# Kernel tuning notes

Measured on AMD Instinct MI355X. Metric: run time of the kernel, lower is better.

Reference implementation:

```python
import jax, jax.numpy as jnp
import numpy as np

B = 1048576  # batch
A = 3        # number of actors in the ensemble


def _linear_params(key, out_d, in_d):
    """Stacked-over-actors torch.nn.Linear-style init: U(-1/sqrt(in), 1/sqrt(in))."""
    k1, k2 = jax.random.split(key)
    s = 1.0 / np.sqrt(in_d)
    W = jax.random.uniform(k1, (A, out_d, in_d), minval=-s, maxval=s, dtype=jnp.float32)
    b = jax.random.uniform(k2, (A, out_d), minval=-s, maxval=s, dtype=jnp.float32)
    return W, b


def setup_inputs() -> dict:
    key = jax.random.key(0)
    ks = jax.random.split(key, 10)
    spatial = jax.random.normal(ks[0], (B, 3, 9), dtype=jnp.float32)
    car_stats = jax.random.normal(ks[1], (B, 4), dtype=jnp.float32)  # unused by the model
    Wmx, bmx = _linear_params(ks[2], 10, 6)
    Wnx, bnx = _linear_params(ks[3], 10, 3)
    Wmy, bmy = _linear_params(ks[4], 10, 6)
    Wny, bny = _linear_params(ks[5], 10, 3)
    Wmz, bmz = _linear_params(ks[6], 5, 6)
    Wnz, bnz = _linear_params(ks[7], 5, 3)
    Wlin, blin = _linear_params(ks[8], 25, 25)
    Wout, bout = _linear_params(ks[9], 15, 25)
    return {
        "spatial": spatial, "car_stats": car_stats,
        "Wmx": Wmx, "bmx": bmx, "Wnx": Wnx, "bnx": bnx,
        "Wmy": Wmy, "bmy": bmy, "Wny": Wny, "bny": bny,
        "Wmz": Wmz, "bmz": bmz, "Wnz": Wnz, "bnz": bnz,
        "Wlin": Wlin, "blin": blin, "Wout": Wout, "bout": bout,
    }


def reference(spatial, car_stats,
              Wmx, bmx, Wnx, bnx,
              Wmy, bmy, Wny, bny,
              Wmz, bmz, Wnz, bnz,
              Wlin, blin, Wout, bout):
    # SimpleSpatialInput vectorized over the actor axis 'a':
    # (Linear(6->size)(s[:, :6])) * (Linear(3->size)(s[:, 6:9]))
    def proc(s, Wm, bm, Wn, bn):
        m = jnp.einsum('bi,aoi->bao', s[:, :6], Wm) + bm   # [B, A, size]
        n = jnp.einsum('bi,aoi->bao', s[:, 6:9], Wn) + bn  # [B, A, size]
        return m * n

    px = proc(spatial[:, 0], Wmx, bmx, Wnx, bnx)  # [B, A, 10]
    py = proc(spatial[:, 1], Wmy, bmy, Wny, bny)  # [B, A, 10]
    pz = proc(spatial[:, 2], Wmz, bmz, Wnz, bnz)  # [B, A, 5]
    ps = jnp.concatenate([px, py, pz], axis=-1)   # [B, A, 25]

    h = jnp.einsum('bad,aod->bao', ps, Wlin) + blin  # [B, A, 25]
    h = h / (1.0 + jnp.abs(h))                       # Softsign
    out = jnp.einsum('bad,aod->bao', h, Wout) + bout # [B, A, 15]

    result = jnp.transpose(out, (0, 2, 1))           # [B, 15, A] (stack dim=2)
    multiplier = jax.nn.softmax(result[:, 9, :], axis=1)  # [B, A]
    # stack of result[:, i] * multiplier over i=0..8, cumsum over actors,
    # take last -> plain weighted sum over the actor axis.
    return jnp.einsum('boa,ba->bo', result[:, :9, :], multiplier)  # [B, 9]
```

## Files before the change

### kernel.cpp

```cpp
#include <hip/hip_runtime.h>


typedef _Float16 half8  __attribute__((ext_vector_type(8)));
typedef float    floatx4 __attribute__((ext_vector_type(4)));

#define NFRAG 21
#define FRAG_HALFS (NFRAG * 512)
#define TPB 16

__global__ __launch_bounds__(256) void prep_frags(
    const float* __restrict__ Wmx, const float* __restrict__ bmx,
    const float* __restrict__ Wnx, const float* __restrict__ bnx,
    const float* __restrict__ Wmy, const float* __restrict__ bmy,
    const float* __restrict__ Wny, const float* __restrict__ bny,
    const float* __restrict__ Wmz, const float* __restrict__ bmz,
    const float* __restrict__ Wnz, const float* __restrict__ bnz,
    const float* __restrict__ Wlin, const float* __restrict__ blin,
    const float* __restrict__ Wout, const float* __restrict__ bout,
    _Float16* __restrict__ frag)
{
    int i = threadIdx.x + blockIdx.x * blockDim.x;
    if (i >= FRAG_HALFS) return;
    int f = i >> 9, rem = i & 511;
    int lane = rem >> 3, j = rem & 7;
    int q = lane >> 4, m = lane & 15;
    int a = f / 7, idx = f % 7;
    float v = 0.f;
    if (idx < 4) {
        int c = m + ((idx & 1) ? 16 : 0);
        int k = 8 * q + j;
        bool npart = (idx >= 2);
        if (c < 10) {
            if (!npart) { if (k < 6)             v = Wmx[(a*10 + c)*6 + k];
                          else if (k == 27)      v = bmx[a*10 + c]; }
            else        { if (k >= 6 && k < 9)   v = Wnx[(a*10 + c)*3 + (k-6)];
                          else if (k == 27)      v = bnx[a*10 + c]; }
        } else if (c < 20) {
            if (!npart) { if (k >= 9 && k < 15)  v = Wmy[(a*10 + c-10)*6 + (k-9)];
                          else if (k == 27)      v = bmy[a*10 + c-10]; }
            else        { if (k >= 15 && k < 18) v = Wny[(a*10 + c-10)*3 + (k-15)];
                          else if (k == 27)      v = bny[a*10 + c-10]; }
        } else if (c < 25) {
            if (!npart) { if (k >= 18 && k < 24) v = Wmz[(a*5 + c-20)*6 + (k-18)];
                          else if (k == 27)      v = bmz[a*5 + c-20]; }
            else        { if (k >= 24 && k < 27) v = Wnz[(a*5 + c-20)*3 + (k-24)];
                          else if (k == 27)      v = bnz[a*5 + c-20]; }
        }
    } else if (idx < 6) {
        int o  = m + ((idx == 5) ? 16 : 0);
        int kc = 16 * (j >> 2) + 4 * q + (j & 3);
        if (o < 25) {
            if (kc < 25)       v = Wlin[(a*25 + o)*25 + kc];
            else if (kc == 25) v = blin[a*25 + o];
        }
    } else {
        int ko = 16 * (j >> 2) + 4 * q + (j & 3);
        if (m < 10) {
            if (ko < 25)       v = Wout[(a*15 + m)*25 + ko];
            else if (ko == 25) v = bout[a*15 + m];
        }
    }
    frag[(size_t)f * 512 + lane * 8 + j] = (_Float16)v;
}

__global__ __launch_bounds__(256) void actor_mfma(
    const float* __restrict__ spatial,
    const _Float16* __restrict__ frag,
    float* __restrict__ out)
{
    __shared__ float lds_o[4 * 144];

    const int t = threadIdx.x;
    const int lane = t & 63, w = t >> 6;
    const int q = lane >> 4, e = lane & 15;
    const size_t b0 = (size_t)blockIdx.x * (64 * TPB);

    half8 F[NFRAG];
    #pragma unroll
    for (int f = 0; f < NFRAG; ++f)
        F[f] = *(const half8*)(frag + (size_t)f * 512 + lane * 8);
    #pragma unroll
    for (int f = 0; f < NFRAG; ++f)
        asm volatile("" : "+v"(F[f]));

    const float* sbase = spatial + (b0 + (size_t)(w * 16 + e)) * 27 + 8 * q;
    float* const ldso = lds_o + w * 144;
    const floatx4 z = {0.f, 0.f, 0.f, 0.f};

    auto loadT = [&](float (&dst)[8], int tt) {
        const float* s_ = sbase + (size_t)tt * (64 * 27);
        #pragma unroll
        for (int j = 0; j < 8; ++j) {
            int k = 8 * q + j;
            float v = (k == 27) ? 1.f : 0.f;
            if (k < 27) v = s_[j];
            dst[j] = v;
        }
    };

    auto tileCompute = [&](const float (&cur)[8], int tt) {
        half8 Bs;
        #pragma unroll
        for (int j = 0; j < 8; ++j) Bs[j] = (_Float16)cur[j];

        floatx4 oacc[3];
        #pragma unroll
        for (int a = 0; a < 3; ++a) {
            const int fb = a * 7;
            half8 P;
            {
                floatx4 M0 = __builtin_amdgcn_mfma_f32_16x16x32_f16(F[fb+0], Bs, z, 0,0,0);
                floatx4 N0 = __builtin_amdgcn_mfma_f32_16x16x32_f16(F[fb+2], Bs, z, 0,0,0);
                #pragma unroll
                for (int r = 0; r < 4; ++r) P[r] = (_Float16)(M0[r] * N0[r]);
            }
            {
                floatx4 M1 = __builtin_amdgcn_mfma_f32_16x16x32_f16(F[fb+1], Bs, z, 0,0,0);
                floatx4 N1 = __builtin_amdgcn_mfma_f32_16x16x32_f16(F[fb+3], Bs, z, 0,0,0);
                #pragma unroll
                for (int r = 0; r < 4; ++r) P[4 + r] = (_Float16)(M1[r] * N1[r]);
            }
            if (q == 2) P[5] = (_Float16)1.f;

            floatx4 H0 = __builtin_amdgcn_mfma_f32_16x16x32_f16(F[fb+4], P, z, 0,0,0);
            floatx4 H1 = __builtin_amdgcn_mfma_f32_16x16x32_f16(F[fb+5], P, z, 0,0,0);

            half8 Hh;
            #pragma unroll
            for (int r = 0; r < 4; ++r) {
                float v0 = H0[r];
                Hh[r]     = (_Float16)(v0 * __builtin_amdgcn_rcpf(1.0f + fabsf(v0)));
                float v1 = H1[r];
                Hh[4 + r] = (_Float16)(v1 * __builtin_amdgcn_rcpf(1.0f + fabsf(v1)));
            }
            if (q == 2) Hh[5] = (_Float16)1.f;

            oacc[a] = __builtin_amdgcn_mfma_f32_16x16x32_f16(F[fb+6], Hh, z, 0,0,0);
        }

        const int src9 = 32 + e;
        float g0 = __shfl(oacc[0][1], src9, 64);
        float g1 = __shfl(oacc[1][1], src9, 64);
        float g2 = __shfl(oacc[2][1], src9, 64);
        float mx = fmaxf(g0, fmaxf(g1, g2));
        float e0 = __expf(g0 - mx);
        float e1 = __expf(g1 - mx);
        float e2 = __expf(g2 - mx);
        float inv = __builtin_amdgcn_rcpf(e0 + e1 + e2);
        e0 *= inv; e1 *= inv; e2 *= inv;

        float res[4];
        #pragma unroll
        for (int r = 0; r < 4; ++r)
            res[r] = oacc[0][r] * e0 + oacc[1][r] * e1 + oacc[2][r] * e2;

        if (q < 2) {
            #pragma unroll
            for (int r = 0; r < 4; ++r) ldso[e * 9 + 4 * q + r] = res[r];
        } else if (q == 2) {
            ldso[e * 9 + 8] = res[0];
        }
        if (lane < 36) {
            float4 v = *(const float4*)(ldso + lane * 4);
            *(float4*)(out + (b0 + (size_t)tt * 64 + w * 16) * 9 + lane * 4) = v;
        }
    };

    float sA[8], sB[8];
    loadT(sA, 0);
    for (int tt = 0; tt < TPB; tt += 2) {
        loadT(sB, tt + 1);
        tileCompute(sA, tt);
        if (tt + 2 < TPB) loadT(sA, tt + 2);
        tileCompute(sB, tt + 1);
    }
}

extern "C" void kernel_launch(void* const* d_in, const int* in_sizes, int n_in,
                              void* d_out, int out_size, void* d_ws, size_t ws_size,
                              hipStream_t stream) {
    const float* spatial = (const float*)d_in[0];
    const float* Wmx  = (const float*)d_in[2];
    const float* bmx  = (const float*)d_in[3];
    const float* Wnx  = (const float*)d_in[4];
    const float* bnx  = (const float*)d_in[5];
    const float* Wmy  = (const float*)d_in[6];
    const float* bmy  = (const float*)d_in[7];
    const float* Wny  = (const float*)d_in[8];
    const float* bny  = (const float*)d_in[9];
    const float* Wmz  = (const float*)d_in[10];
    const float* bmz  = (const float*)d_in[11];
    const float* Wnz  = (const float*)d_in[12];
    const float* bnz  = (const float*)d_in[13];
    const float* Wlin = (const float*)d_in[14];
    const float* blin = (const float*)d_in[15];
    const float* Wout = (const float*)d_in[16];
    const float* bout = (const float*)d_in[17];
    float* out = (float*)d_out;

    _Float16* frag = (_Float16*)d_ws;

    prep_frags<<<dim3(42), dim3(256), 0, stream>>>(
        Wmx, bmx, Wnx, bnx, Wmy, bmy, Wny, bny, Wmz, bmz, Wnz, bnz,
        Wlin, blin, Wout, bout, frag);

    const int nb = in_sizes[0] / 27;
    dim3 grid(nb / (64 * TPB));
    actor_mfma<<<grid, dim3(256), 0, stream>>>(spatial, frag, out);
}
```

Measured before the change: 260.1 us.

## Stage weight fragments in LDS instead of registers and shrink tiles per block

The 21 weight fragments now live in shared memory: each block copies them cooperatively, and every wave reads them with LDS loads per MFMA instead of holding 84 VGPRs of fragments. This frees registers to raise occupancy and hide global-load latency. To compensate, tiles per block drop from 16 to 4, giving four times as many blocks. The cost is extra LDS traffic per tile and a per-block fragment copy plus barrier that is amortised over fewer tiles.

Result: faster. 241.2 us (-7.3%).

```diff
diff --git a/kernel.cpp b/kernel.cpp
--- a/kernel.cpp
+++ b/kernel.cpp
@@ -6,7 +6,7 @@
 
 #define NFRAG 21
 #define FRAG_HALFS (NFRAG * 512)
-#define TPB 16
+#define TPB 4
 
 __global__ __launch_bounds__(256) void prep_frags(
     const float* __restrict__ Wmx, const float* __restrict__ bmx,
@@ -68,33 +68,42 @@
     const _Float16* __restrict__ frag,
     float* __restrict__ out)
 {
-    __shared__ float lds_o[4 * 144];
+    __shared__ _Float16 lds_f[FRAG_HALFS];
+    __shared__ float    lds_o[4 * 144];
 
     const int t = threadIdx.x;
     const int lane = t & 63, w = t >> 6;
     const int q = lane >> 4, e = lane & 15;
     const size_t b0 = (size_t)blockIdx.x * (64 * TPB);
 
-    half8 F[NFRAG];
+    {
+        const float4* gf = (const float4*)frag;
+        float4* df = (float4*)lds_f;
+        #pragma unroll
+        for (int k = 0; k < 6; ++k) {
+            int idx = t + k * 256;
+            if (idx < 1344) df[idx] = gf[idx];
+        }
+    }
+
+    const float* sbase = spatial + (b0 + (size_t)(w * 16 + e)) * 27 + 8 * q;
+    float vbase[8];
     #pragma unroll
-    for (int f = 0; f < NFRAG; ++f)
-        F[f] = *(const half8*)(frag + (size_t)f * 512 + lane * 8);
-    #pragma unroll
-    for (int f = 0; f < NFRAG; ++f)
-        asm volatile("" : "+v"(F[f]));
-
-    const float* sbase = spatial + (b0 + (size_t)(w * 16 + e)) * 27 + 8 * q;
+    for (int j = 0; j < 8; ++j) vbase[j] = ((8 * q + j) == 27) ? 1.f : 0.f;
+
     float* const ldso = lds_o + w * 144;
     const floatx4 z = {0.f, 0.f, 0.f, 0.f};
 
+    __syncthreads();
+
+    int fo = lane;
+
     auto loadT = [&](float (&dst)[8], int tt) {
         const float* s_ = sbase + (size_t)tt * (64 * 27);
         #pragma unroll
         for (int j = 0; j < 8; ++j) {
             int k = 8 * q + j;
-            float v = (k == 27) ? 1.f : 0.f;
-            if (k < 27) v = s_[j];
-            dst[j] = v;
+            dst[j] = (k < 27) ? s_[j] : vbase[j];
         }
     };
 
@@ -106,24 +115,26 @@
         floatx4 oacc[3];
         #pragma unroll
         for (int a = 0; a < 3; ++a) {
+            asm volatile("" : "+v"(fo));
+            const half8* fp = (const half8*)lds_f + fo;
             const int fb = a * 7;
             half8 P;
             {
-                floatx4 M0 = __builtin_amdgcn_mfma_f32_16x16x32_f16(F[fb+0], Bs, z, 0,0,0);
-                floatx4 N0 = __builtin_amdgcn_mfma_f32_16x16x32_f16(F[fb+2], Bs, z, 0,0,0);
+                floatx4 M0 = __builtin_amdgcn_mfma_f32_16x16x32_f16(fp[(fb+0)*64], Bs, z, 0,0,0);
+                floatx4 N0 = __builtin_amdgcn_mfma_f32_16x16x32_f16(fp[(fb+2)*64], Bs, z, 0,0,0);
                 #pragma unroll
                 for (int r = 0; r < 4; ++r) P[r] = (_Float16)(M0[r] * N0[r]);
             }
             {
-                floatx4 M1 = __builtin_amdgcn_mfma_f32_16x16x32_f16(F[fb+1], Bs, z, 0,0,0);
-                floatx4 N1 = __builtin_amdgcn_mfma_f32_16x16x32_f16(F[fb+3], Bs, z, 0,0,0);
+                floatx4 M1 = __builtin_amdgcn_mfma_f32_16x16x32_f16(fp[(fb+1)*64], Bs, z, 0,0,0);
+                floatx4 N1 = __builtin_amdgcn_mfma_f32_16x16x32_f16(fp[(fb+3)*64], Bs, z, 0,0,0);
                 #pragma unroll
                 for (int r = 0; r < 4; ++r) P[4 + r] = (_Float16)(M1[r] * N1[r]);
             }
             if (q == 2) P[5] = (_Float16)1.f;
 
-            floatx4 H0 = __builtin_amdgcn_mfma_f32_16x16x32_f16(F[fb+4], P, z, 0,0,0);
-            floatx4 H1 = __builtin_amdgcn_mfma_f32_16x16x32_f16(F[fb+5], P, z, 0,0,0);
+            floatx4 H0 = __builtin_amdgcn_mfma_f32_16x16x32_f16(fp[(fb+4)*64], P, z, 0,0,0);
+            floatx4 H1 = __builtin_amdgcn_mfma_f32_16x16x32_f16(fp[(fb+5)*64], P, z, 0,0,0);
 
             half8 Hh;
             #pragma unroll
@@ -135,7 +146,7 @@
             }
             if (q == 2) Hh[5] = (_Float16)1.f;
 
-            oacc[a] = __builtin_amdgcn_mfma_f32_16x16x32_f16(F[fb+6], Hh, z, 0,0,0);
+            oacc[a] = __builtin_amdgcn_mfma_f32_16x16x32_f16(fp[(fb+6)*64], Hh, z, 0,0,0);
         }
 
         const int src9 = 32 + e;
```
